# Kernel tuning notes

Measured on AMD Instinct MI355X. Metric: run time of the kernel, lower is better.

Reference implementation:

```python
import jax, jax.numpy as jnp
import numpy as np

N = 4096          # batch of anchors
D = 128           # embedding dim
M = 4             # instances per class (balanced batch) -> 3 positives per anchor
MARGIN = 1.0
INF = jnp.float32(1e30)


def setup_inputs() -> dict:
    key = jax.random.key(0)
    inputs = jax.random.normal(key, (N, D), dtype=jnp.float32)
    targets = (jnp.arange(N, dtype=jnp.int32) // M).astype(jnp.int32)
    return {"inputs": inputs, "targets": targets}


def _forward(inputs, targets, key):
    n = inputs.shape[0]
    k_pos = M - 1            # positives per anchor (and multinomial draw count)
    k_neg = n - M            # negatives per anchor

    # euclidean_dist: ||xi||^2 + ||xj||^2 - 2 xi.xj, clamped and sqrt'ed
    sq = jnp.sum(inputs * inputs, axis=1)
    dist = sq[:, None] + sq[None, :] - 2.0 * (inputs @ inputs.T)
    dist = jnp.sqrt(jnp.clip(dist, 1e-12, None))

    same = targets[:, None] == targets[None, :]
    eye = jnp.eye(n, dtype=bool)
    pos_mask = same & ~eye
    neg_mask = ~same

    # balanced batch -> exactly k_pos positives / k_neg negatives per row;
    # push non-members to +inf and sort (original sorts pos/neg pairs anyway)
    pos_sorted = jnp.sort(jnp.where(pos_mask, dist, INF), axis=1)[:, :k_pos]  # [n, 3]
    neg_sorted = jnp.sort(jnp.where(neg_mask, dist, INF), axis=1)[:, :k_neg]  # [n, n-M]

    pos3 = pos_sorted[:, :3]  # pos_pair[:3]

    # GaussDistribution over the (sorted) negative row
    neg_mean = jnp.mean(neg_sorted, axis=1, keepdims=True)
    neg_std = jnp.sqrt(jnp.mean((neg_sorted - neg_mean) ** 2, axis=1, keepdims=True))
    # prob = exp((x-mean)^2 / (2 std^2)); use log-weights for Gumbel-top-k
    log_prob = (neg_sorted - neg_mean) ** 2 / (2.0 * neg_std ** 2)

    # multinomial without replacement == top-k of log_prob + Gumbel noise
    g = jax.random.gumbel(key, neg_sorted.shape, dtype=jnp.float32)
    _, idx = jax.lax.top_k(log_prob + g, k_pos)                 # [n, 3]
    sampled = jnp.take_along_axis(neg_sorted, idx, axis=1)      # [n, 3]

    # masked_select(neg_pair < pos_pair[-1] + 0.05) -> boolean keep mask
    kept = sampled < (pos3[:, -1:] + 0.05)
    cnt = jnp.sum(kept, axis=1)
    any_kept = cnt > 0

    # pos_loss = 0.5*mean(log(1+exp(-2*(margin - pos))))
    pos_loss = 0.5 * jnp.mean(jax.nn.softplus(-2.0 * (MARGIN - pos3)), axis=1)
    # neg_loss = 0.05*mean over kept of log(1+exp(20*(margin - neg)))
    neg_terms = jax.nn.softplus(20.0 * (MARGIN - sampled))
    neg_loss = 0.05 * jnp.sum(jnp.where(kept, neg_terms, 0.0), axis=1) / jnp.maximum(cnt, 1)

    row_loss = jnp.where(any_kept, pos_loss + neg_loss, 0.0)
    loss = jnp.sum(row_loss) / n

    # err: pos_pair[0] < neg_pair[0] - 0.1 (first kept sampled negative)
    first_idx = jnp.argmax(kept, axis=1)
    neg0 = jnp.take_along_axis(sampled, first_idx[:, None], axis=1)[:, 0]
    err = jnp.sum((any_kept & (pos3[:, 0] < neg0 - 0.1)).astype(jnp.float32))
    prec = 1.0 - err / n

    pos_d = jnp.mean(pos_sorted)
    neg_d = jnp.mean(neg_sorted)
    return loss, prec, pos_d, neg_d


def reference(inputs, targets):
    key = jax.random.key(42)  # fixed sampling key (torch.multinomial analogue)
    return _forward(inputs, targets, key)
```

## Files before the change

### kernel.cpp

```cpp
#include <hip/hip_runtime.h>
#include <stdint.h>

#define NROW 4096
#define NDIM 128
#define KNEG 4092
#define INF_VAL 1e30f
#define BUCKETS 2048
#define DISTBLKS 1024
#define DSTR 68

typedef __attribute__((ext_vector_type(8))) short short8;
typedef __attribute__((ext_vector_type(4))) float f32x4;

__device__ __forceinline__ uint32_t rotl32(uint32_t v, int d) {
  return __builtin_rotateleft32(v, (unsigned)d);
}

__device__ __forceinline__ void threefry2x32(uint32_t x0, uint32_t x1,
                                             uint32_t& y0, uint32_t& y1) {
  const uint32_t k0 = 0u, k1 = 42u;
  const uint32_t k2 = 0x1BD11BDAu ^ k0 ^ k1;
  uint32_t v0 = x0 + k0, v1 = x1 + k1;
#define TF_R(r) v0 += v1; v1 = rotl32(v1, r); v1 ^= v0;
  TF_R(13) TF_R(15) TF_R(26) TF_R(6)
  v0 += k1; v1 += k2 + 1u;
  TF_R(17) TF_R(29) TF_R(16) TF_R(24)
  v0 += k2; v1 += k0 + 2u;
  TF_R(13) TF_R(15) TF_R(26) TF_R(6)
  v0 += k0; v1 += k1 + 3u;
  TF_R(17) TF_R(29) TF_R(16) TF_R(24)
  v0 += k1; v1 += k2 + 4u;
  TF_R(13) TF_R(15) TF_R(26) TF_R(6)
  v0 += k2; v1 += k0 + 5u;
#undef TF_R
  y0 = v0; y1 = v1;
}

__device__ __forceinline__ float gumbel_ref(uint32_t f) {
  uint32_t y0, y1;
  threefry2x32(0u, f, y0, y1);
  uint32_t m = y1 >> 9;
  float fm = (float)m;
  float nl = fmaf(-0.69314718f, __log2f(fm), 15.942385f);
  if (m == 0u) nl = 87.33655f;
  return -0.69314718f * __log2f(nl);
}

__device__ __forceinline__ float softplus_ref(float x) {
  return fmaxf(x, 0.0f) + log1pf(expf(-fabsf(x)));
}

__device__ __forceinline__ ushort f2h(float f) {
  _Float16 h = (_Float16)f;
  return *(ushort*)&h;
}
__device__ __forceinline__ float h2f(ushort u) {
  _Float16 h = *(_Float16*)&u;
  return (float)h;
}
__device__ __forceinline__ float bf2f(ushort u) {
  return __uint_as_float(((uint32_t)u) << 16);
}
__device__ __forceinline__ ushort f2bf(float f) {
  uint32_t u = __float_as_uint(f);
  u += 0x7fffu + ((u >> 16) & 1u);
  return (ushort)(u >> 16);
}

__device__ __forceinline__ ushort gumbel_h(uint32_t f) {
  return f2h(gumbel_ref(f));
}

__device__ __forceinline__ int bucket_code(ushort code) {
  return min(max((int)code - 0x4000, 0), BUCKETS - 1);
}

__device__ __forceinline__ uint32_t fkey(float f) {
  uint32_t b = __float_as_uint(f);
  return b ^ ((uint32_t)((int32_t)b >> 31) | 0x80000000u);
}

__device__ __forceinline__ void ins3(uint64_t v, uint64_t& t0, uint64_t& t1,
                                     uint64_t& t2) {
  bool c0 = v > t0, c1 = v > t1, c2 = v > t2;
  t2 = c1 ? t1 : (c2 ? v : t2);
  t1 = c0 ? t0 : (c1 ? v : t1);
  t0 = c0 ? v : t0;
}

__device__ __forceinline__ void merge3(uint64_t& a0, uint64_t& a1, uint64_t& a2,
                                       uint64_t b0, uint64_t b1, uint64_t b2) {
  bool sw = b0 > a0;
  uint64_t n0 = sw ? b0 : a0, m0 = sw ? a0 : b0;
  uint64_t n1 = sw ? b1 : a1, m1 = sw ? a1 : b1;
  uint64_t n2 = sw ? b2 : a2;
  a0 = n0;
  bool c = n1 >= m0;
  a1 = c ? n1 : m0;
  uint64_t u = c ? n2 : n1;
  uint64_t w = c ? m0 : m1;
  a2 = (u > w) ? u : w;
}

__global__ __launch_bounds__(256) void prep_kernel(const float* __restrict__ X,
                                                   float* __restrict__ sq,
                                                   ushort* __restrict__ Xbf) {
  const int tid = threadIdx.x;
  const int lane = tid & 63;
  const int i = (blockIdx.x << 2) + (tid >> 6);
  float2 v = ((const float2*)(X + (size_t)i * NDIM))[lane];
  float s = v.x * v.x + v.y * v.y;
  for (int o = 32; o > 0; o >>= 1) s += __shfl_down(s, o);
  if (lane == 0) sq[i] = s;
  ushort2 h;
  h.x = f2bf(v.x);
  h.y = f2bf(v.y);
  ((ushort2*)(Xbf + (size_t)i * NDIM))[lane] = h;
}

__global__ __launch_bounds__(256) void dist_kernel(const ushort* __restrict__ Xbf,
                                                   const float* __restrict__ sq,
                                                   ushort* __restrict__ distb) {
  __shared__ ushort Als[128 * DSTR];
  __shared__ ushort Bls[128 * DSTR];
  const int tid = threadIdx.x;
  const int bi = blockIdx.x >> 5, bj = blockIdx.x & 31;
  const int wave = tid >> 6, lane = tid & 63;
  const int q = lane >> 4, ln = lane & 15;
  const ushort* Ag = Xbf + (size_t)bi * 128 * NDIM;
  const ushort* Bg = Xbf + (size_t)bj * 128 * NDIM;

  f32x4 acc[8][2];
#pragma unroll
  for (int mt = 0; mt < 8; ++mt)
#pragma unroll
    for (int nt = 0; nt < 2; ++nt) acc[mt][nt] = (f32x4){0.f, 0.f, 0.f, 0.f};

  for (int kh = 0; kh < 2; ++kh) {
    if (kh) __syncthreads();
#pragma unroll
    for (int t = 0; t < 4; ++t) {
      int c = tid + 256 * t;
      int r = c >> 3, k8 = (c & 7) << 3;
      *(short8*)&Als[r * DSTR + k8] =
          *(const short8*)(Ag + (size_t)r * NDIM + kh * 64 + k8);
      *(short8*)&Bls[r * DSTR + k8] =
          *(const short8*)(Bg + (size_t)r * NDIM + kh * 64 + k8);
    }
    __syncthreads();
#pragma unroll
    for (int k0 = 0; k0 < 64; k0 += 32) {
      int kf = k0 + q * 8;
      short8 a[8], b[2];
#pragma unroll
      for (int mt = 0; mt < 8; ++mt)
        a[mt] = *(const short8*)&Als[(mt * 16 + ln) * DSTR + kf];
#pragma unroll
      for (int nt = 0; nt < 2; ++nt)
        b[nt] = *(const short8*)&Bls[(wave * 32 + 2 * ln + nt) * DSTR + kf];
#pragma unroll
      for (int mt = 0; mt < 8; ++mt)
#pragma unroll
        for (int nt = 0; nt < 2; ++nt)
          acc[mt][nt] = __builtin_amdgcn_mfma_f32_16x16x32_bf16(
              a[mt], b[nt], acc[mt][nt], 0, 0, 0);
    }
  }

  const int jcol = bj * 128 + wave * 32 + 2 * ln;
  float sqj0 = sq[jcol], sqj1 = sq[jcol + 1];
#pragma unroll
  for (int mt = 0; mt < 8; ++mt) {
    int ibase = bi * 128 + mt * 16 + q * 4;
#pragma unroll
    for (int r = 0; r < 4; ++r) {
      int i = ibase + r;
      float sqi = sq[i];
      float dx = sqrtf(fmaxf(sqi + sqj0 - 2.0f * acc[mt][0][r], 1e-12f));
      float dy = sqrtf(fmaxf(sqi + sqj1 - 2.0f * acc[mt][1][r], 1e-12f));
      uint32_t pack = ((uint32_t)f2bf(dy) << 16) | (uint32_t)f2bf(dx);
      *(uint32_t*)(distb + (size_t)i * NROW + jcol) = pack;
    }
  }
}

__global__ __launch_bounds__(256) void row_kernel(const ushort* __restrict__ distb,
                                                  float4* __restrict__ part) {
  __shared__ alignas(16) ushort sortc[NROW];
  __shared__ alignas(16) int base[BUCKETS];
  __shared__ float wredf[8];
  __shared__ int wtot[4];
  __shared__ float s_pos[3];
  __shared__ int s_selp[3];

  uint64_t* cand = (uint64_t*)base;

  const int i = blockIdx.x;
  const int tid = threadIdx.x;
  const int lane = tid & 63, wid = tid >> 6;
  const ushort* row = distb + (size_t)i * NROW;
  const int gbase = i & ~3;
  const uint32_t fbase = (uint32_t)i * (uint32_t)KNEG;

  {
    int4* b4 = (int4*)base;
    b4[tid] = (int4){0, 0, 0, 0};
    b4[tid + 256] = (int4){0, 0, 0, 0};
  }

  short8 r0 = *(const short8*)(row + tid * 16);
  short8 r1 = *(const short8*)(row + tid * 16 + 8);

  uint32_t gpack[8];
#pragma unroll
  for (int j = 0; j < 8; ++j) {
    uint32_t lo = (uint32_t)gumbel_h(fbase + (uint32_t)(tid + 512 * j));
    uint32_t hi = (uint32_t)gumbel_h(fbase + (uint32_t)(tid + 512 * j + 256));
    gpack[j] = lo | (hi << 16);
  }

  ushort cd[16];
  float x[16];
#pragma unroll
  for (int k = 0; k < 8; ++k) {
    cd[k] = (ushort)r0[k];     x[k] = bf2f(cd[k]);
    cd[8 + k] = (ushort)r1[k]; x[8 + k] = bf2f(cd[8 + k]);
  }

  if (tid == (gbase >> 4)) {
    float p[3]; int np = 0;
#pragma unroll
    for (int qq = 0; qq < 4; ++qq) {
      int j = gbase + qq;
      if (j != i) p[np++] = x[j & 15];
    }
    float a = p[0], b = p[1], c = p[2], t_;
    if (a > b) { t_ = a; a = b; b = t_; }
    if (b > c) { t_ = b; b = c; c = t_; }
    if (a > b) { t_ = a; a = b; b = t_; }
    s_pos[0] = a; s_pos[1] = b; s_pos[2] = c;
  }

#pragma unroll
  for (int qq = 0; qq < 16; ++qq) {
    int j = tid * 16 + qq;
    if ((j >> 2) == (i >> 2)) { x[qq] = INF_VAL; cd[qq] = 0x7F80u; }
  }
  __syncthreads();

  int bkt[16];
  int ord[16];
  float ls = 0.f;
#pragma unroll
  for (int qq = 0; qq < 16; ++qq) {
    bkt[qq] = bucket_code(cd[qq]);
    ord[qq] = atomicAdd(&base[bkt[qq]], 1);
    if (x[qq] < 1e29f) ls += x[qq];
  }
  for (int o = 32; o > 0; o >>= 1) ls += __shfl_down(ls, o);
  if (lane == 0) wredf[wid] = ls;
  __syncthreads();
  const float negsum = wredf[0] + wredf[1] + wredf[2] + wredf[3];
  const float mean = negsum / (float)KNEG;

  int c8[8]; int lsum = 0;
#pragma unroll
  for (int qq = 0; qq < 8; ++qq) {
    int t_ = base[tid * 8 + qq];
    c8[qq] = lsum; lsum += t_;
  }
  float ls2 = 0.f;
#pragma unroll
  for (int qq = 0; qq < 16; ++qq)
    if (x[qq] < 1e29f) { float z = x[qq] - mean; ls2 += z * z; }
  int incl = lsum;
  for (int off = 1; off < 64; off <<= 1) {
    int o = __shfl_up(incl, off);
    if (lane >= off) incl += o;
  }
  for (int o = 32; o > 0; o >>= 1) ls2 += __shfl_down(ls2, o);
  if (lane == 63) wtot[wid] = incl;
  if (lane == 0) wredf[4 + wid] = ls2;
  __syncthreads();
  const float var = (wredf[4] + wredf[5] + wredf[6] + wredf[7]) / (float)KNEG;
  const float stdv = sqrtf(var);
  const float rdenom = __frcp_rn(2.0f * stdv * stdv);
  int excl = incl - lsum;
#pragma unroll
  for (int w = 0; w < 4; ++w) if (w < wid) excl += wtot[w];
#pragma unroll
  for (int qq = 0; qq < 8; ++qq) base[tid * 8 + qq] = excl + c8[qq];
  __syncthreads();

#pragma unroll
  for (int qq = 0; qq < 16; ++qq) {
    int p = base[bkt[qq]] + ord[qq];
    sortc[p] = cd[qq];
  }
  __syncthreads();

  uint64_t t0 = 0, t1 = 0, t2 = 0;
#pragma unroll
  for (int qq = 0; qq < 16; ++qq) {
    int p = tid + 256 * qq;
    float xv = bf2f(sortc[p]);
    if (p < KNEG) {
      float z = xv - mean;
      uint32_t gp = gpack[qq >> 1];
      ushort gc = (qq & 1) ? (ushort)(gp >> 16) : (ushort)(gp & 0xffffu);
      float gv = h2f(gc);
      float sv = fmaf(z * z, rdenom, gv);
      uint64_t v = ((uint64_t)fkey(sv) << 32) | (uint32_t)(8192 - p);
      ins3(v, t0, t1, t2);
    }
  }
  cand[tid * 3 + 0] = t0;
  cand[tid * 3 + 1] = t1;
  cand[tid * 3 + 2] = t2;
  __syncthreads();

  if (wid == 0) {
    uint64_t a0 = 0, a1 = 0, a2 = 0;
#pragma unroll
    for (int k = 0; k < 12; ++k) {
      uint64_t v = cand[lane + 64 * k];
      ins3(v, a0, a1, a2);
    }
#pragma unroll
    for (int m = 32; m > 0; m >>= 1) {
      uint64_t b0 = __shfl_xor((unsigned long long)a0, m);
      uint64_t b1 = __shfl_xor((unsigned long long)a1, m);
      uint64_t b2 = __shfl_xor((unsigned long long)a2, m);
      merge3(a0, a1, a2, b0, b1, b2);
    }
    if (lane == 0) {
      s_selp[0] = 8192 - (int)(uint32_t)a0;
      s_selp[1] = 8192 - (int)(uint32_t)a1;
      s_selp[2] = 8192 - (int)(uint32_t)a2;
    }
  }
  __syncthreads();

  if (tid == 0) {
    float p0 = s_pos[0], p1 = s_pos[1], p2 = s_pos[2];
    float thr = p2 + 0.05f;
    float samp[3]; bool kept[3]; int cnt = 0;
#pragma unroll
    for (int t = 0; t < 3; ++t) {
      samp[t] = bf2f(sortc[s_selp[t]]);
      kept[t] = samp[t] < thr;
      cnt += kept[t] ? 1 : 0;
    }
    bool any = cnt > 0;
    float pos_loss = 0.5f *
        (softplus_ref(-2.0f * (1.0f - p0)) + softplus_ref(-2.0f * (1.0f - p1)) +
         softplus_ref(-2.0f * (1.0f - p2))) / 3.0f;
    float nsum = 0.0f;
#pragma unroll
    for (int t = 0; t < 3; ++t)
      if (kept[t]) nsum += softplus_ref(20.0f * (1.0f - samp[t]));
    float neg_loss = 0.05f * nsum / (float)(cnt > 0 ? cnt : 1);
    float row_loss = any ? (pos_loss + neg_loss) : 0.0f;
    int first = kept[0] ? 0 : (kept[1] ? 1 : (kept[2] ? 2 : 0));
    float neg0 = samp[first];
    float errv = (any && (p0 < neg0 - 0.1f)) ? 1.0f : 0.0f;
    float4 pr;
    pr.x = row_loss; pr.y = errv; pr.z = p0 + p1 + p2; pr.w = negsum;
    part[i] = pr;
  }
}

__global__ __launch_bounds__(256) void reduce_kernel(const float4* __restrict__ part,
                                                     float* __restrict__ out) {
  __shared__ double wsum[4][4];
  const int tid = threadIdx.x;
  const int lane = tid & 63, wid = tid >> 6;
  double s0 = 0.0, s1 = 0.0, s2 = 0.0, s3 = 0.0;
  for (int k = tid; k < NROW; k += 256) {
    float4 v = part[k];
    s0 += (double)v.x; s1 += (double)v.y; s2 += (double)v.z; s3 += (double)v.w;
  }
  for (int o = 32; o > 0; o >>= 1) {
    s0 += __shfl_down(s0, o); s1 += __shfl_down(s1, o);
    s2 += __shfl_down(s2, o); s3 += __shfl_down(s3, o);
  }
  if (lane == 0) {
    wsum[wid][0] = s0; wsum[wid][1] = s1; wsum[wid][2] = s2; wsum[wid][3] = s3;
  }
  __syncthreads();
  if (tid == 0) {
    double a0 = wsum[0][0] + wsum[1][0] + wsum[2][0] + wsum[3][0];
    double a1 = wsum[0][1] + wsum[1][1] + wsum[2][1] + wsum[3][1];
    double a2 = wsum[0][2] + wsum[1][2] + wsum[2][2] + wsum[3][2];
    double a3 = wsum[0][3] + wsum[1][3] + wsum[2][3] + wsum[3][3];
    out[0] = (float)(a0 / (double)NROW);
    out[1] = (float)(1.0 - a1 / (double)NROW);
    out[2] = (float)(a2 / ((double)NROW * 3.0));
    out[3] = (float)(a3 / ((double)NROW * (double)KNEG));
  }
}

extern "C" void kernel_launch(void* const* d_in, const int* in_sizes, int n_in,
                              void* d_out, int out_size, void* d_ws, size_t ws_size,
                              hipStream_t stream) {
  (void)in_sizes; (void)n_in; (void)out_size; (void)ws_size;
  const float* X = (const float*)d_in[0];
  float* out = (float*)d_out;
  char* ws = (char*)d_ws;

  ushort* distb = (ushort*)ws;
  size_t off = (size_t)NROW * NROW * sizeof(ushort);
  float* sq = (float*)(ws + off);            off += NROW * sizeof(float);
  ushort* Xbf = (ushort*)(ws + off);         off += (size_t)NROW * NDIM * sizeof(ushort);
  float4* part = (float4*)(ws + off);        off += (size_t)NROW * sizeof(float4);

  prep_kernel<<<NROW / 4, 256, 0, stream>>>(X, sq, Xbf);
  dist_kernel<<<DISTBLKS, 256, 0, stream>>>(Xbf, sq, distb);
  row_kernel<<<NROW, 256, 0, stream>>>(distb, part);
  reduce_kernel<<<1, 256, 0, stream>>>(part, out);
}
```

Baseline: 150.5 us.

## Skip sorted-row scatter; score elements in place using their rank

Stops scattering each row into a sorted shared-memory array. Instead, each thread computes every element's sorted position from the bucket prefix sums and scores it directly, carrying the distance value alongside the top-3 keys. Gumbel noise is now computed at the rank position inside the scoring loop rather than precomputed, which removes one shared-memory scatter, a barrier and the re-read of the sorted row. The trade-off is extra register pressure from the paired values and a longer reduction when merging payloads through the wave shuffles.

After: 150.8 us. Within noise of the previous version (+0.2%).

```diff
diff --git a/kernel.cpp b/kernel.cpp
--- a/kernel.cpp
+++ b/kernel.cpp
@@ -67,8 +67,8 @@
   return (ushort)(u >> 16);
 }
 
-__device__ __forceinline__ ushort gumbel_h(uint32_t f) {
-  return f2h(gumbel_ref(f));
+__device__ __forceinline__ float gumbel_h2f(uint32_t f) {
+  return h2f(f2h(gumbel_ref(f)));
 }
 
 __device__ __forceinline__ int bucket_code(ushort code) {
@@ -80,26 +80,35 @@
   return b ^ ((uint32_t)((int32_t)b >> 31) | 0x80000000u);
 }
 
-__device__ __forceinline__ void ins3(uint64_t v, uint64_t& t0, uint64_t& t1,
-                                     uint64_t& t2) {
+__device__ __forceinline__ void ins3p(uint64_t v, float s,
+                                      uint64_t& t0, float& s0,
+                                      uint64_t& t1, float& s1,
+                                      uint64_t& t2, float& s2) {
   bool c0 = v > t0, c1 = v > t1, c2 = v > t2;
-  t2 = c1 ? t1 : (c2 ? v : t2);
-  t1 = c0 ? t0 : (c1 ? v : t1);
-  t0 = c0 ? v : t0;
-}
-
-__device__ __forceinline__ void merge3(uint64_t& a0, uint64_t& a1, uint64_t& a2,
-                                       uint64_t b0, uint64_t b1, uint64_t b2) {
+  t2 = c1 ? t1 : (c2 ? v : t2); s2 = c1 ? s1 : (c2 ? s : s2);
+  t1 = c0 ? t0 : (c1 ? v : t1); s1 = c0 ? s0 : (c1 ? s : s1);
+  t0 = c0 ? v : t0;             s0 = c0 ? s : s0;
+}
+
+__device__ __forceinline__ void merge3p(uint64_t& a0, float& p0,
+                                        uint64_t& a1, float& p1,
+                                        uint64_t& a2, float& p2,
+                                        uint64_t b0, float q0,
+                                        uint64_t b1, float q1,
+                                        uint64_t b2, float q2) {
   bool sw = b0 > a0;
-  uint64_t n0 = sw ? b0 : a0, m0 = sw ? a0 : b0;
-  uint64_t n1 = sw ? b1 : a1, m1 = sw ? a1 : b1;
-  uint64_t n2 = sw ? b2 : a2;
-  a0 = n0;
-  bool c = n1 >= m0;
-  a1 = c ? n1 : m0;
-  uint64_t u = c ? n2 : n1;
-  uint64_t w = c ? m0 : m1;
-  a2 = (u > w) ? u : w;
+  uint64_t n0 = sw ? b0 : a0; float n0p = sw ? q0 : p0;
+  uint64_t m0 = sw ? a0 : b0; float m0p = sw ? p0 : q0;
+  uint64_t n1 = sw ? b1 : a1; float n1p = sw ? q1 : p1;
+  uint64_t m1 = sw ? a1 : b1; float m1p = sw ? p1 : q1;
+  uint64_t n2 = sw ? b2 : a2; float n2p = sw ? q2 : p2;
+  a0 = n0; p0 = n0p;
+  bool c = n1 > m0;
+  a1 = c ? n1 : m0;  p1 = c ? n1p : m0p;
+  uint64_t u = c ? n2 : n1; float up = c ? n2p : n1p;
+  uint64_t w = c ? m0 : m1; float wp = c ? m0p : m1p;
+  bool d = u > w;
+  a2 = d ? u : w; p2 = d ? up : wp;
 }
 
 __global__ __launch_bounds__(256) void prep_kernel(const float* __restrict__ X,
@@ -186,12 +195,12 @@
 
 __global__ __launch_bounds__(256) void row_kernel(const ushort* __restrict__ distb,
                                                   float4* __restrict__ part) {
-  __shared__ alignas(16) ushort sortc[NROW];
   __shared__ alignas(16) int base[BUCKETS];
+  __shared__ alignas(16) float candx[768];
   __shared__ float wredf[8];
   __shared__ int wtot[4];
   __shared__ float s_pos[3];
-  __shared__ int s_selp[3];
+  __shared__ float s_selx[3];
 
   uint64_t* cand = (uint64_t*)base;
 
@@ -211,14 +220,6 @@
   short8 r0 = *(const short8*)(row + tid * 16);
   short8 r1 = *(const short8*)(row + tid * 16 + 8);
 
-  uint32_t gpack[8];
-#pragma unroll
-  for (int j = 0; j < 8; ++j) {
-    uint32_t lo = (uint32_t)gumbel_h(fbase + (uint32_t)(tid + 512 * j));
-    uint32_t hi = (uint32_t)gumbel_h(fbase + (uint32_t)(tid + 512 * j + 256));
-    gpack[j] = lo | (hi << 16);
-  }
-
   ushort cd[16];
   float x[16];
 #pragma unroll
@@ -292,51 +293,52 @@
   for (int qq = 0; qq < 8; ++qq) base[tid * 8 + qq] = excl + c8[qq];
   __syncthreads();
 
+  uint64_t t0 = 0, t1 = 0, t2 = 0;
+  float t0x = 0.f, t1x = 0.f, t2x = 0.f;
 #pragma unroll
   for (int qq = 0; qq < 16; ++qq) {
-    int p = base[bkt[qq]] + ord[qq];
-    sortc[p] = cd[qq];
-  }
-  __syncthreads();
-
-  uint64_t t0 = 0, t1 = 0, t2 = 0;
-#pragma unroll
-  for (int qq = 0; qq < 16; ++qq) {
-    int p = tid + 256 * qq;
-    float xv = bf2f(sortc[p]);
-    if (p < KNEG) {
+    if (x[qq] < 1e29f) {
+      int p = base[bkt[qq]] + ord[qq];
+      float xv = x[qq];
       float z = xv - mean;
-      uint32_t gp = gpack[qq >> 1];
-      ushort gc = (qq & 1) ? (ushort)(gp >> 16) : (ushort)(gp & 0xffffu);
-      float gv = h2f(gc);
+      float gv = gumbel_h2f(fbase + (uint32_t)p);
       float sv = fmaf(z * z, rdenom, gv);
       uint64_t v = ((uint64_t)fkey(sv) << 32) | (uint32_t)(8192 - p);
-      ins3(v, t0, t1, t2);
-    }
-  }
-  cand[tid * 3 + 0] = t0;
-  cand[tid * 3 + 1] = t1;
-  cand[tid * 3 + 2] = t2;
+      ins3p(v, xv, t0, t0x, t1, t1x, t2, t2x);
+    }
+  }
+  __syncthreads();
+
+  cand[tid * 3 + 0] = t0; candx[tid * 3 + 0] = t0x;
+  cand[tid * 3 + 1] = t1; candx[tid * 3 + 1] = t1x;
+  cand[tid * 3 + 2] = t2; candx[tid * 3 + 2] = t2x;
   __syncthreads();
 
   if (wid == 0) {
     uint64_t a0 = 0, a1 = 0, a2 = 0;
+    int i0 = 0, i1 = 0, i2 = 0;
 #pragma unroll
     for (int k = 0; k < 12; ++k) {
-      uint64_t v = cand[lane + 64 * k];
-      ins3(v, a0, a1, a2);
-    }
+      int idx = lane + 64 * k;
+      uint64_t v = cand[idx];
+      bool c0 = v > a0, c1 = v > a1, c2 = v > a2;
+      a2 = c1 ? a1 : (c2 ? v : a2); i2 = c1 ? i1 : (c2 ? idx : i2);
+      a1 = c0 ? a0 : (c1 ? v : a1); i1 = c0 ? i0 : (c1 ? idx : i1);
+      a0 = c0 ? v : a0;             i0 = c0 ? idx : i0;
+    }
+    float p0 = candx[i0], p1 = candx[i1], p2 = candx[i2];
 #pragma unroll
     for (int m = 32; m > 0; m >>= 1) {
       uint64_t b0 = __shfl_xor((unsigned long long)a0, m);
       uint64_t b1 = __shfl_xor((unsigned long long)a1, m);
       uint64_t b2 = __shfl_xor((unsigned long long)a2, m);
-      merge3(a0, a1, a2, b0, b1, b2);
+      float q0 = __shfl_xor(p0, m);
+      float q1 = __shfl_xor(p1, m);
+      float q2 = __shfl_xor(p2, m);
+      merge3p(a0, p0, a1, p1, a2, p2, b0, q0, b1, q1, b2, q2);
     }
     if (lane == 0) {
-      s_selp[0] = 8192 - (int)(uint32_t)a0;
-      s_selp[1] = 8192 - (int)(uint32_t)a1;
-      s_selp[2] = 8192 - (int)(uint32_t)a2;
+      s_selx[0] = p0; s_selx[1] = p1; s_selx[2] = p2;
     }
   }
   __syncthreads();
@@ -347,7 +349,7 @@
     float samp[3]; bool kept[3]; int cnt = 0;
 #pragma unroll
     for (int t = 0; t < 3; ++t) {
-      samp[t] = bf2f(sortc[s_selp[t]]);
+      samp[t] = s_selx[t];
       kept[t] = samp[t] < thr;
       cnt += kept[t] ? 1 : 0;
     }
```
